# Performance work log

Measured on AMD Instinct MI355X. Metric: run time of the kernel, lower is better.

Reference implementation:

```python
import jax, jax.numpy as jnp
import numpy as np

B, M, N = 32, 512, 128
HH, WW = 128, 128

def setup_inputs() -> dict:
    key = jax.random.key(0)
    kx, kl = jax.random.split(key)
    x = jax.random.normal(kx, (B, M, N), dtype=jnp.float32)
    # non-overlapping locations per batch (module requires no overlap):
    # take first M entries of a random permutation of the H*W flat grid
    keys = jax.random.split(kl, B)
    flat = jax.vmap(lambda k: jax.random.permutation(k, HH * WW)[:M])(keys)  # (B, M)
    location = jnp.stack([flat // WW, flat % WW], axis=-1).astype(jnp.int64)  # (B, M, 2) as (y, x)
    return {"x": x, "location": location, "H": HH, "W": WW}

def reference(x, location, H, W):
    Bb, Mm, Nn = x.shape
    flat_idx = location[..., 0] * W + location[..., 1]          # (B, M)
    out = jnp.zeros((Bb, H * W, Nn), dtype=x.dtype)
    out = out.at[jnp.arange(Bb)[:, None], flat_idx].set(x)       # scatter all B*M entities at once
    return out.transpose(0, 2, 1).reshape(Bb, Nn, H, W)          # (B, N, H, W)
```

## Files before the change

kernel.cpp:

```cpp
#include <hip/hip_runtime.h>

constexpr int B  = 32;
constexpr int M  = 512;
constexpr int N  = 128;
constexpr int H  = 128;
constexpr int W  = 128;
constexpr int HW = H * W;
constexpr int PLANE = N * HW;

typedef float f4 __attribute__((ext_vector_type(4)));
typedef int   i4 __attribute__((ext_vector_type(4)));

__global__ void init_inv_kernel(int* __restrict__ inv) {
    int t = blockIdx.x * blockDim.x + threadIdx.x;
    i4 v = {-1, -1, -1, -1};
    reinterpret_cast<i4*>(inv)[t] = v;
}

__global__ void build_inv_kernel(const int* __restrict__ loc, int* __restrict__ inv) {
    int tid = blockIdx.x * blockDim.x + threadIdx.x;
    int b = tid >> 9;
    int y = loc[tid * 2 + 0];
    int x = loc[tid * 2 + 1];
    inv[b * HW + y * W + x] = tid & (M - 1);
}

__global__ void gather_out_kernel(const float* __restrict__ x,
                                  const int* __restrict__ inv,
                                  float* __restrict__ out) {
    int t  = blockIdx.x * blockDim.x + threadIdx.x;
    int p  = (t & 4095) << 2;
    int nb = (t >> 12) & 15;
    int b  = t >> 16;
    int n0 = nb << 3;

    const i4 iv = *reinterpret_cast<const i4*>(inv + (b << 14) + p);
    const float* xb = x + (b << 16);
    float* ob = out + (b << 21) + (n0 << 14) + p;

    const f4 zero = {0.f, 0.f, 0.f, 0.f};

    #pragma unroll
    for (int h = 0; h < 2; ++h) {
        const int nh = n0 + (h << 2);
        f4 x0 = (iv[0] >= 0) ? *reinterpret_cast<const f4*>(xb + (iv[0] << 7) + nh) : zero;
        f4 x1 = (iv[1] >= 0) ? *reinterpret_cast<const f4*>(xb + (iv[1] << 7) + nh) : zero;
        f4 x2 = (iv[2] >= 0) ? *reinterpret_cast<const f4*>(xb + (iv[2] << 7) + nh) : zero;
        f4 x3 = (iv[3] >= 0) ? *reinterpret_cast<const f4*>(xb + (iv[3] << 7) + nh) : zero;

        float* o = ob + (h << 16);
        #pragma unroll
        for (int j = 0; j < 4; ++j) {
            f4 v = {x0[j], x1[j], x2[j], x3[j]};
            __builtin_nontemporal_store(v, reinterpret_cast<f4*>(o + (j << 14)));
        }
    }
}

extern "C" void kernel_launch(void* const* d_in, const int* in_sizes, int n_in,
                              void* d_out, int out_size, void* d_ws, size_t ws_size,
                              hipStream_t stream) {
    const float* x   = (const float*)d_in[0];
    const int*   loc = (const int*)d_in[1];
    float* out = (float*)d_out;
    int*   inv = (int*)d_ws;

    init_inv_kernel<<<(B * HW / 4) / 256, 256, 0, stream>>>(inv);
    build_inv_kernel<<<(B * M) / 256, 256, 0, stream>>>(loc, inv);
    gather_out_kernel<<<(B * PLANE / 32) / 256, 256, 0, stream>>>(x, inv, out);
}
```

Measured before the change: 59.39 us.

## Widen per-thread channel work and use a zero page instead of predicated loads

Each thread now produces 32 channels for four pixels instead of 8, over a 2048-block grid. The inverse index is loaded once and turned into four base pointers. Empty pixels point at a small zeroed page in the workspace, so the loads carry no branches. Non-temporal stores are replaced by ordinary stores; this trades fewer blocks and less index reloading for more registers per thread and possible cache pollution from the 256 MB output.

```diff
diff --git a/kernel.cpp b/kernel.cpp
--- a/kernel.cpp
+++ b/kernel.cpp
@@ -7,14 +7,20 @@
 constexpr int W  = 128;
 constexpr int HW = H * W;
 constexpr int PLANE = N * HW;
+constexpr size_t INV_BYTES = (size_t)B * HW * 4;
+constexpr size_t ZP_FLOATS = 128;
 
 typedef float f4 __attribute__((ext_vector_type(4)));
 typedef int   i4 __attribute__((ext_vector_type(4)));
 
-__global__ void init_inv_kernel(int* __restrict__ inv) {
+__global__ void init_inv_kernel(int* __restrict__ inv, float* __restrict__ zpage) {
     int t = blockIdx.x * blockDim.x + threadIdx.x;
     i4 v = {-1, -1, -1, -1};
     reinterpret_cast<i4*>(inv)[t] = v;
+    if (t < (int)(ZP_FLOATS / 4)) {
+        f4 z = {0.f, 0.f, 0.f, 0.f};
+        reinterpret_cast<f4*>(zpage)[t] = z;
+    }
 }
 
 __global__ void build_inv_kernel(const int* __restrict__ loc, int* __restrict__ inv) {
@@ -27,32 +33,37 @@
 
 __global__ void gather_out_kernel(const float* __restrict__ x,
                                   const int* __restrict__ inv,
+                                  const float* __restrict__ zpage,
                                   float* __restrict__ out) {
-    int t  = blockIdx.x * blockDim.x + threadIdx.x;
-    int p  = (t & 4095) << 2;
-    int nb = (t >> 12) & 15;
-    int b  = t >> 16;
-    int n0 = nb << 3;
+    int bid = blockIdx.x;
+    int b  = bid >> 6;
+    int nc = (bid >> 4) & 3;
+    int pc = bid & 15;
+    int p  = (pc << 10) + ((int)threadIdx.x << 2);
+    int n0 = nc << 5;
 
     const i4 iv = *reinterpret_cast<const i4*>(inv + (b << 14) + p);
-    const float* xb = x + (b << 16);
+    const float* xb = x + (b << 16) + n0;
+
+    const float* a0 = (iv[0] >= 0) ? (xb + (iv[0] << 7)) : zpage;
+    const float* a1 = (iv[1] >= 0) ? (xb + (iv[1] << 7)) : zpage;
+    const float* a2 = (iv[2] >= 0) ? (xb + (iv[2] << 7)) : zpage;
+    const float* a3 = (iv[3] >= 0) ? (xb + (iv[3] << 7)) : zpage;
+
     float* ob = out + (b << 21) + (n0 << 14) + p;
 
-    const f4 zero = {0.f, 0.f, 0.f, 0.f};
+    #pragma unroll
+    for (int it = 0; it < 8; ++it) {
+        f4 x0 = *reinterpret_cast<const f4*>(a0 + (it << 2));
+        f4 x1 = *reinterpret_cast<const f4*>(a1 + (it << 2));
+        f4 x2 = *reinterpret_cast<const f4*>(a2 + (it << 2));
+        f4 x3 = *reinterpret_cast<const f4*>(a3 + (it << 2));
 
-    #pragma unroll
-    for (int h = 0; h < 2; ++h) {
-        const int nh = n0 + (h << 2);
-        f4 x0 = (iv[0] >= 0) ? *reinterpret_cast<const f4*>(xb + (iv[0] << 7) + nh) : zero;
-        f4 x1 = (iv[1] >= 0) ? *reinterpret_cast<const f4*>(xb + (iv[1] << 7) + nh) : zero;
-        f4 x2 = (iv[2] >= 0) ? *reinterpret_cast<const f4*>(xb + (iv[2] << 7) + nh) : zero;
-        f4 x3 = (iv[3] >= 0) ? *reinterpret_cast<const f4*>(xb + (iv[3] << 7) + nh) : zero;
-
-        float* o = ob + (h << 16);
+        float* o = ob + (it << 16);
         #pragma unroll
         for (int j = 0; j < 4; ++j) {
             f4 v = {x0[j], x1[j], x2[j], x3[j]};
-            __builtin_nontemporal_store(v, reinterpret_cast<f4*>(o + (j << 14)));
+            *reinterpret_cast<f4*>(o + (j << 14)) = v;
         }
     }
 }
@@ -64,8 +75,9 @@
     const int*   loc = (const int*)d_in[1];
     float* out = (float*)d_out;
     int*   inv = (int*)d_ws;
+    float* zpage = (float*)((char*)d_ws + INV_BYTES);
 
-    init_inv_kernel<<<(B * HW / 4) / 256, 256, 0, stream>>>(inv);
+    init_inv_kernel<<<(B * HW / 4) / 256, 256, 0, stream>>>(inv, zpage);
     build_inv_kernel<<<(B * M) / 256, 256, 0, stream>>>(loc, inv);
-    gather_out_kernel<<<(B * PLANE / 32) / 256, 256, 0, stream>>>(x, inv, out);
+    gather_out_kernel<<<2048, 256, 0, stream>>>(x, inv, zpage, out);
 }
```

Measured after the change: 58.84 us. Within noise of the previous version (-0.9%).

## Fuse inverse-map build into gather kernel using per-block shared-memory map

Applied to the files above, without the earlier changes.

Replaces the three-kernel pipeline (global inverse-map init, build, gather) with one kernel. Each block loads its batch's locations and builds a 1024-pixel inverse map in LDS, then writes 64 channels of output per thread group. This removes two launches and the global workspace traffic. In exchange, every block redundantly reads all 512 locations, loads are issued unconditionally with zero-masking, and the nontemporal stores become plain stores.

```diff
diff --git a/kernel.cpp b/kernel.cpp
--- a/kernel.cpp
+++ b/kernel.cpp
@@ -11,48 +11,64 @@
 typedef float f4 __attribute__((ext_vector_type(4)));
 typedef int   i4 __attribute__((ext_vector_type(4)));
 
-__global__ void init_inv_kernel(int* __restrict__ inv) {
-    int t = blockIdx.x * blockDim.x + threadIdx.x;
-    i4 v = {-1, -1, -1, -1};
-    reinterpret_cast<i4*>(inv)[t] = v;
-}
+__global__ __launch_bounds__(256, 4)
+void fused_scatter_kernel(const float* __restrict__ x,
+                          const int* __restrict__ loc,
+                          float* __restrict__ out) {
+    __shared__ int lmap[1024];
 
-__global__ void build_inv_kernel(const int* __restrict__ loc, int* __restrict__ inv) {
-    int tid = blockIdx.x * blockDim.x + threadIdx.x;
-    int b = tid >> 9;
-    int y = loc[tid * 2 + 0];
-    int x = loc[tid * 2 + 1];
-    inv[b * HW + y * W + x] = tid & (M - 1);
-}
+    const int tid = threadIdx.x;
+    const int bid = blockIdx.x;
+    const int b  = bid >> 5;
+    const int pc = (bid >> 1) & 15;
+    const int n0 = (bid & 1) << 6;
+    const int p0 = pc << 10;
 
-__global__ void gather_out_kernel(const float* __restrict__ x,
-                                  const int* __restrict__ inv,
-                                  float* __restrict__ out) {
-    int t  = blockIdx.x * blockDim.x + threadIdx.x;
-    int p  = (t & 4095) << 2;
-    int nb = (t >> 12) & 15;
-    int b  = t >> 16;
-    int n0 = nb << 3;
+    const i4 lv = *reinterpret_cast<const i4*>(loc + (b << 10) + (tid << 2));
 
-    const i4 iv = *reinterpret_cast<const i4*>(inv + (b << 14) + p);
-    const float* xb = x + (b << 16);
-    float* ob = out + (b << 21) + (n0 << 14) + p;
+    i4 neg = {-1, -1, -1, -1};
+    *reinterpret_cast<i4*>(&lmap[tid << 2]) = neg;
+    __syncthreads();
 
-    const f4 zero = {0.f, 0.f, 0.f, 0.f};
+    const int f0 = (lv[0] << 7) + lv[1] - p0;
+    const int f1 = (lv[2] << 7) + lv[3] - p0;
+    if ((unsigned)f0 < 1024u) lmap[f0] = (tid << 1);
+    if ((unsigned)f1 < 1024u) lmap[f1] = (tid << 1) + 1;
+    __syncthreads();
+
+    const i4 iv = *reinterpret_cast<const i4*>(&lmap[tid << 2]);
+    const bool v0 = iv[0] >= 0, v1 = iv[1] >= 0, v2 = iv[2] >= 0, v3 = iv[3] >= 0;
+
+    const float* xb = x + (b << 16) + n0;
+    const float* a0 = xb + ((v0 ? iv[0] : 0) << 7);
+    const float* a1 = xb + ((v1 ? iv[1] : 0) << 7);
+    const float* a2 = xb + ((v2 ? iv[2] : 0) << 7);
+    const float* a3 = xb + ((v3 ? iv[3] : 0) << 7);
+
+    float* ob = out + (b << 21) + (n0 << 14) + p0 + (tid << 2);
 
     #pragma unroll
-    for (int h = 0; h < 2; ++h) {
-        const int nh = n0 + (h << 2);
-        f4 x0 = (iv[0] >= 0) ? *reinterpret_cast<const f4*>(xb + (iv[0] << 7) + nh) : zero;
-        f4 x1 = (iv[1] >= 0) ? *reinterpret_cast<const f4*>(xb + (iv[1] << 7) + nh) : zero;
-        f4 x2 = (iv[2] >= 0) ? *reinterpret_cast<const f4*>(xb + (iv[2] << 7) + nh) : zero;
-        f4 x3 = (iv[3] >= 0) ? *reinterpret_cast<const f4*>(xb + (iv[3] << 7) + nh) : zero;
-
-        float* o = ob + (h << 16);
+    for (int g = 0; g < 4; ++g) {
+        f4 xv[4][4];
         #pragma unroll
-        for (int j = 0; j < 4; ++j) {
-            f4 v = {x0[j], x1[j], x2[j], x3[j]};
-            __builtin_nontemporal_store(v, reinterpret_cast<f4*>(o + (j << 14)));
+        for (int it = 0; it < 4; ++it) {
+            const int off = (g << 4) + (it << 2);
+            xv[it][0] = *reinterpret_cast<const f4*>(a0 + off);
+            xv[it][1] = *reinterpret_cast<const f4*>(a1 + off);
+            xv[it][2] = *reinterpret_cast<const f4*>(a2 + off);
+            xv[it][3] = *reinterpret_cast<const f4*>(a3 + off);
+        }
+        #pragma unroll
+        for (int it = 0; it < 4; ++it) {
+            float* o = ob + (((g << 4) + (it << 2)) << 14);
+            #pragma unroll
+            for (int j = 0; j < 4; ++j) {
+                f4 v = {v0 ? xv[it][0][j] : 0.f,
+                        v1 ? xv[it][1][j] : 0.f,
+                        v2 ? xv[it][2][j] : 0.f,
+                        v3 ? xv[it][3][j] : 0.f};
+                *reinterpret_cast<f4*>(o + (j << 14)) = v;
+            }
         }
     }
 }
@@ -63,9 +79,6 @@
     const float* x   = (const float*)d_in[0];
     const int*   loc = (const int*)d_in[1];
     float* out = (float*)d_out;
-    int*   inv = (int*)d_ws;
 
-    init_inv_kernel<<<(B * HW / 4) / 256, 256, 0, stream>>>(inv);
-    build_inv_kernel<<<(B * M) / 256, 256, 0, stream>>>(loc, inv);
-    gather_out_kernel<<<(B * PLANE / 32) / 256, 256, 0, stream>>>(x, inv, out);
+    fused_scatter_kernel<<<1024, 256, 0, stream>>>(x, loc, out);
 }
```

Result: faster. 48.72 us (-18.0%).
